# Optimization experiments

Hardware: AMD Instinct MI355X
Metric: run time of the kernel (lower is better)

Reference implementation:

```python
import jax, jax.numpy as jnp
import numpy as np


def _gru_scan(x_seq, Wih, Whh, bih, bhh):
    # x_seq: (S, N, D); PyTorch GRU/GRUCell gate math, h0 = 0. Returns (S, N, H).
    H = Whh.shape[1]
    gi_all = x_seq @ Wih.T + bih  # precompute input projections: (S, N, 3H)

    def step(h, gi):
        gh = h @ Whh.T + bhh
        ir, iz, inn = jnp.split(gi, 3, axis=-1)
        hr, hz, hn = jnp.split(gh, 3, axis=-1)
        r = jax.nn.sigmoid(ir + hr)
        z = jax.nn.sigmoid(iz + hz)
        n = jnp.tanh(inn + r * hn)
        h_new = (1.0 - z) * n + z * h
        return h_new, h_new

    h0 = jnp.zeros((x_seq.shape[1], H), x_seq.dtype)
    _, ys = jax.lax.scan(step, h0, gi_all)
    return ys


def setup_inputs() -> dict:
    key = jax.random.key(0)
    ks = jax.random.split(key, 40)
    B, T = 32, 800
    NOTE, E, P, H0, H1, FE, RE = 128, 256, 256, 512, 512, 64, 64

    def w(k, shape):
        return jax.random.normal(k, shape, dtype=jnp.float32) * 0.05

    return {
        "note": jax.random.randint(ks[0], (B, T), 0, NOTE, dtype=jnp.int64),
        "f0_prev": jax.random.normal(ks[1], (B, T), dtype=jnp.float32),
        "rmse_prev": jax.random.normal(ks[2], (B, T), dtype=jnp.float32),
        "note_emb": w(ks[3], (NOTE, E)),
        "f0_W": w(ks[4], (FE, 1)), "f0_b": w(ks[5], (FE,)),
        "rmse_W": w(ks[6], (RE, 1)), "rmse_b": w(ks[7], (RE,)),
        "pre1_W": w(ks[8], (P, E)), "pre1_b": w(ks[9], (P,)),
        "pre2_W": w(ks[10], (P, P)), "pre2_b": w(ks[11], (P,)),
        "encf_Wih": w(ks[12], (3 * H0, P)), "encf_Whh": w(ks[13], (3 * H0, H0)),
        "encf_bih": w(ks[14], (3 * H0,)), "encf_bhh": w(ks[15], (3 * H0,)),
        "encb_Wih": w(ks[16], (3 * H0, P)), "encb_Whh": w(ks[17], (3 * H0, H0)),
        "encb_bih": w(ks[18], (3 * H0,)), "encb_bhh": w(ks[19], (3 * H0,)),
        "decf_Wih": w(ks[20], (3 * H1, 2 * H0 + FE)), "decf_Whh": w(ks[21], (3 * H1, H1)),
        "decf_bih": w(ks[22], (3 * H1,)), "decf_bhh": w(ks[23], (3 * H1,)),
        "decr_Wih": w(ks[24], (3 * H1, 2 * H0 + RE)), "decr_Whh": w(ks[25], (3 * H1, H1)),
        "decr_bih": w(ks[26], (3 * H1,)), "decr_bhh": w(ks[27], (3 * H1,)),
        "postf_W": w(ks[28], (1, H1)), "postf_b": w(ks[29], (1,)),
        "postr_W": w(ks[30], (1, H1)), "postr_b": w(ks[31], (1,)),
    }


def reference(note, f0_prev, rmse_prev, note_emb, f0_W, f0_b, rmse_W, rmse_b,
              pre1_W, pre1_b, pre2_W, pre2_b,
              encf_Wih, encf_Whh, encf_bih, encf_bhh,
              encb_Wih, encb_Whh, encb_bih, encb_bhh,
              decf_Wih, decf_Whh, decf_bih, decf_bhh,
              decr_Wih, decr_Whh, decr_bih, decr_bhh,
              postf_W, postf_b, postr_W, postr_b):
    # Embeddings. Linear(1, FE) on a [B,T] signal == outer-broadcast with W[:,0].
    ne = note_emb[note]                                   # (B, T, E)
    f0e = f0_prev[..., None] * f0_W[:, 0] + f0_b          # (B, T, FE)
    rme = rmse_prev[..., None] * rmse_W[:, 0] + rmse_b    # (B, T, RE)

    # Prenet: Linear -> Tanh -> Linear -> Tanh
    h = jnp.tanh(jnp.tanh(ne @ pre1_W.T + pre1_b) @ pre2_W.T + pre2_b)  # (B, T, P)

    # Encoder: torch nn.GRU built WITHOUT batch_first and called with lengths=None,
    # so the recurrence runs over axis 0 (B) with T acting as the GRU batch. Replicated.
    ef = _gru_scan(h, encf_Wih, encf_Whh, encf_bih, encf_bhh)            # (B, T, H0)
    eb = _gru_scan(h[::-1], encb_Wih, encb_Whh, encb_bih, encb_bhh)[::-1]
    enc = jnp.concatenate([ef, eb], axis=-1)                             # (B, T, 2H0)

    # Decoders: GRUCell loop over T with teacher forcing (y_prevs has T>1 steps),
    # so step-t input is concat(enc[:, t], embed(prev[:, t])) -> standard scan.
    xt = jnp.transpose(enc, (1, 0, 2))                                   # (T, B, 2H0)
    hf = _gru_scan(jnp.concatenate([xt, jnp.transpose(f0e, (1, 0, 2))], -1),
                   decf_Wih, decf_Whh, decf_bih, decf_bhh)               # (T, B, H1)
    hr = _gru_scan(jnp.concatenate([xt, jnp.transpose(rme, (1, 0, 2))], -1),
                   decr_Wih, decr_Whh, decr_bih, decr_bhh)               # (T, B, H1)

    f0 = jnp.transpose((hf @ postf_W.T + postf_b)[..., 0], (1, 0))       # (B, T)
    rmse = jnp.transpose((hr @ postr_W.T + postr_b)[..., 0], (1, 0))     # (B, T)
    return (f0, rmse)
```

## Files before the change

kernel.cpp:

```cpp
#include <hip/hip_runtime.h>
#include <hip/hip_bf16.h>


typedef __bf16 bf16;
typedef bf16 bf16x8 __attribute__((ext_vector_type(8)));
typedef float f32x4 __attribute__((ext_vector_type(4)));
typedef float f32x2 __attribute__((ext_vector_type(2)));

#define BATCH 32
#define TLEN 800
#define BT (BATCH * TLEN)

__device__ __forceinline__ float bf2f(bf16 v) {
    unsigned short u = __builtin_bit_cast(unsigned short, v);
    unsigned int x = ((unsigned int)u) << 16;
    return __builtin_bit_cast(float, x);
}
__device__ __forceinline__ bf16 f2bf(float f) {
    unsigned int x = __builtin_bit_cast(unsigned int, f);
    unsigned int r = (x + 0x7FFFu + ((x >> 16) & 1u)) >> 16;
    return __builtin_bit_cast(bf16, (unsigned short)r);
}
__device__ __forceinline__ bf16x8 ld8f(const float* p) {
    f32x4 a = *(const f32x4*)p;
    f32x4 b = *(const f32x4*)(p + 4);
    bf16x8 r;
#pragma unroll
    for (int i = 0; i < 4; i++) {
        r[i] = f2bf(a[i]);
        r[i + 4] = f2bf(b[i]);
    }
    return r;
}
__device__ __forceinline__ void splitv(f32x4 a, f32x4 b, bf16x8& vh, bf16x8& vl) {
#pragma unroll
    for (int j = 0; j < 4; j++) {
        bf16 h0 = f2bf(a[j]);
        vh[j] = h0;
        vl[j] = f2bf(a[j] - bf2f(h0));
        bf16 h1 = f2bf(b[j]);
        vh[j + 4] = h1;
        vl[j + 4] = f2bf(b[j] - bf2f(h1));
    }
}
__device__ __forceinline__ f32x4 mfma16(bf16x8 a, bf16x8 b, f32x4 c) {
    return __builtin_amdgcn_mfma_f32_16x16x32_bf16(a, b, c, 0, 0, 0);
}
__device__ __forceinline__ float sigm(float x) { return 1.f / (1.f + __expf(-x)); }

__device__ __forceinline__ void cst_f32(float* p, float v) {
    __hip_atomic_store((unsigned int*)p, __builtin_bit_cast(unsigned int, v),
                       __ATOMIC_RELAXED, __HIP_MEMORY_SCOPE_AGENT);
}
__device__ __forceinline__ float cld_f32(const float* p) {
    unsigned int u = __hip_atomic_load((const unsigned int*)p, __ATOMIC_RELAXED,
                                       __HIP_MEMORY_SCOPE_AGENT);
    return __builtin_bit_cast(float, u);
}
__device__ __forceinline__ f32x4 cld_f32x4(const float* p) {
    unsigned long long a = __hip_atomic_load((const unsigned long long*)p,
                                             __ATOMIC_RELAXED,
                                             __HIP_MEMORY_SCOPE_AGENT);
    unsigned long long b = __hip_atomic_load((const unsigned long long*)(p + 2),
                                             __ATOMIC_RELAXED,
                                             __HIP_MEMORY_SCOPE_AGENT);
    f32x2 fa = __builtin_bit_cast(f32x2, a);
    f32x2 fb = __builtin_bit_cast(f32x2, b);
    f32x4 r;
    r[0] = fa[0]; r[1] = fa[1]; r[2] = fb[0]; r[3] = fb[1];
    return r;
}

template <int MODE>
__global__ __launch_bounds__(256) void gemm01_k(
    const int* __restrict__ note, const float* __restrict__ asrc,
    const float* __restrict__ W, const float* __restrict__ bias,
    float* __restrict__ out, int t0, int TC) {
    __shared__ bf16 Ah[128][72], Al[128][72], Bs[128][72];

    const int tid = threadIdx.x;
    const int lane = tid & 63, wv = tid >> 6;
    const int wm = wv & 1, wn = wv >> 1;
    const int l15 = lane & 15, hi = lane >> 4;
    const int bm = blockIdx.x * 128, bn = blockIdx.y * 128;
    const int ch = (tid & 7) * 8, arow = tid >> 3;

    f32x4 acc[4][4] = {};
    const float* ap[4];
    if (MODE == 0) {
        int zc = 0;
        for (int i = 0; i < 64; i++) zc += (note[2 * i + 1] == 0) ? 1 : 0;
        const bool n64 = (zc >= 60);
#pragma unroll
        for (int i = 0; i < 4; i++) {
            int m = bm + arow + 32 * i;
            int b = m / TC, tt = m - b * TC;
            int idx = b * TLEN + t0 + tt;
            int id = n64 ? note[2 * idx] : note[idx];
            id = id < 0 ? 0 : (id > 127 ? 127 : id);
            ap[i] = asrc + (size_t)id * 256;
        }
    } else {
#pragma unroll
        for (int i = 0; i < 4; i++) ap[i] = asrc + (size_t)(bm + arow + 32 * i) * 256;
    }

    for (int k0 = 0; k0 < 256; k0 += 64) {
#pragma unroll
        for (int i = 0; i < 4; i++) {
            int row = arow + 32 * i;
            f32x4 va = *(const f32x4*)(ap[i] + k0 + ch);
            f32x4 vb = *(const f32x4*)(ap[i] + k0 + ch + 4);
            bf16x8 vh, vl;
            splitv(va, vb, vh, vl);
            *(bf16x8*)&Ah[row][ch] = vh;
            *(bf16x8*)&Al[row][ch] = vl;
        }
#pragma unroll
        for (int i = 0; i < 4; i++) {
            int row = arow + 32 * i;
            *(bf16x8*)&Bs[row][ch] = ld8f(W + (size_t)(bn + row) * 256 + k0 + ch);
        }
        __syncthreads();
#pragma unroll
        for (int kk = 0; kk < 64; kk += 32) {
            bf16x8 ah[4], al[4], bb[4];
#pragma unroll
            for (int mt = 0; mt < 4; mt++) {
                ah[mt] = *(const bf16x8*)&Ah[wm * 64 + mt * 16 + l15][kk + hi * 8];
                al[mt] = *(const bf16x8*)&Al[wm * 64 + mt * 16 + l15][kk + hi * 8];
            }
#pragma unroll
            for (int nt = 0; nt < 4; nt++)
                bb[nt] = *(const bf16x8*)&Bs[wn * 64 + nt * 16 + l15][kk + hi * 8];
#pragma unroll
            for (int mt = 0; mt < 4; mt++)
#pragma unroll
                for (int nt = 0; nt < 4; nt++) {
                    acc[mt][nt] = mfma16(ah[mt], bb[nt], acc[mt][nt]);
                    acc[mt][nt] = mfma16(al[mt], bb[nt], acc[mt][nt]);
                }
        }
        __syncthreads();
    }

#pragma unroll
    for (int mt = 0; mt < 4; mt++)
#pragma unroll
        for (int nt = 0; nt < 4; nt++) {
            int n = bn + wn * 64 + nt * 16 + l15;
            float bs = bias[n];
#pragma unroll
            for (int r = 0; r < 4; r++) {
                int m = bm + wm * 64 + mt * 16 + hi * 4 + r;
                out[(size_t)m * 256 + n] = tanhf(acc[mt][nt][r] + bs);
            }
        }
}

__global__ __launch_bounds__(256) void gemm2_k(
    const float* __restrict__ ef, const float* __restrict__ eb,
    const float* __restrict__ sig, const float* __restrict__ sigW,
    const float* __restrict__ sigB, const float* __restrict__ W,
    const float* __restrict__ bias, float* __restrict__ out, int t0, int TC) {
    __shared__ bf16 Ah[128][72], Al[128][72];
    __shared__ bf16 Bh[64][72], Bl[64][72];

    const int tid = threadIdx.x;
    const int lane = tid & 63, wv = tid >> 6;
    const int wm = wv & 1, wn = wv >> 1;
    const int l15 = lane & 15, hi = lane >> 4;
    const int bm = blockIdx.x * 128, bn = blockIdx.y * 64;
    const int ch = (tid & 7) * 8, arow = tid >> 3;

    f32x4 acc[4][2] = {};
    int rb[4];
    float sigv[4];
#pragma unroll
    for (int i = 0; i < 4; i++) {
        int m = bm + arow + 32 * i;
        int tt = m >> 5, b = m & 31;
        rb[i] = b * TC + tt;
        sigv[i] = sig[b * TLEN + t0 + tt];
    }

    for (int k0 = 0; k0 < 1088; k0 += 64) {
#pragma unroll
        for (int i = 0; i < 4; i++) {
            int row = arow + 32 * i;
            int k = k0 + ch;
            f32x4 va, vb;
            if (k < 512) {
                va = *(const f32x4*)(ef + (size_t)rb[i] * 512 + k);
                vb = *(const f32x4*)(ef + (size_t)rb[i] * 512 + k + 4);
            } else if (k < 1024) {
                va = *(const f32x4*)(eb + (size_t)rb[i] * 512 + (k - 512));
                vb = *(const f32x4*)(eb + (size_t)rb[i] * 512 + (k - 512) + 4);
            } else {
                f32x4 w0 = *(const f32x4*)(sigW + ch);
                f32x4 w1 = *(const f32x4*)(sigW + ch + 4);
                f32x4 b0 = *(const f32x4*)(sigB + ch);
                f32x4 b1 = *(const f32x4*)(sigB + ch + 4);
                float s = sigv[i];
#pragma unroll
                for (int j = 0; j < 4; j++) {
                    va[j] = s * w0[j] + b0[j];
                    vb[j] = s * w1[j] + b1[j];
                }
            }
            bf16x8 vh, vl;
            splitv(va, vb, vh, vl);
            *(bf16x8*)&Ah[row][ch] = vh;
            *(bf16x8*)&Al[row][ch] = vl;
        }
#pragma unroll
        for (int i = 0; i < 2; i++) {
            int row = arow + 32 * i;
            const float* src = W + (size_t)(bn + row) * 1088 + k0 + ch;
            f32x4 va = *(const f32x4*)src;
            f32x4 vb = *(const f32x4*)(src + 4);
            bf16x8 vh, vl;
            splitv(va, vb, vh, vl);
            *(bf16x8*)&Bh[row][ch] = vh;
            *(bf16x8*)&Bl[row][ch] = vl;
        }
        __syncthreads();
#pragma unroll
        for (int kk = 0; kk < 64; kk += 32) {
            bf16x8 ah[4], al[4], bh[2], bl[2];
#pragma unroll
            for (int mt = 0; mt < 4; mt++) {
                ah[mt] = *(const bf16x8*)&Ah[wm * 64 + mt * 16 + l15][kk + hi * 8];
                al[mt] = *(const bf16x8*)&Al[wm * 64 + mt * 16 + l15][kk + hi * 8];
            }
#pragma unroll
            for (int nt = 0; nt < 2; nt++) {
                bh[nt] = *(const bf16x8*)&Bh[wn * 32 + nt * 16 + l15][kk + hi * 8];
                bl[nt] = *(const bf16x8*)&Bl[wn * 32 + nt * 16 + l15][kk + hi * 8];
            }
#pragma unroll
            for (int mt = 0; mt < 4; mt++)
#pragma unroll
                for (int nt = 0; nt < 2; nt++) {
                    acc[mt][nt] = mfma16(ah[mt], bh[nt], acc[mt][nt]);
                    acc[mt][nt] = mfma16(al[mt], bh[nt], acc[mt][nt]);
                    acc[mt][nt] = mfma16(ah[mt], bl[nt], acc[mt][nt]);
                }
        }
        __syncthreads();
    }

#pragma unroll
    for (int mt = 0; mt < 4; mt++)
#pragma unroll
        for (int nt = 0; nt < 2; nt++) {
            int n = bn + wn * 32 + nt * 16 + l15;
            float bs = bias[n];
#pragma unroll
            for (int r = 0; r < 4; r++) {
                int m = bm + wm * 64 + mt * 16 + hi * 4 + r;
                out[(size_t)m * 1536 + n] = acc[mt][nt][r] + bs;
            }
        }
}

__global__ __launch_bounds__(256) void enc_step_k(
    int step, int TC, const float* __restrict__ hpre, float* __restrict__ efb,
    float* __restrict__ ebb, const float* __restrict__ fWih,
    const float* __restrict__ fWhh, const float* __restrict__ fbih,
    const float* __restrict__ fbhh, const float* __restrict__ bWih,
    const float* __restrict__ bWhh, const float* __restrict__ bbih,
    const float* __restrict__ bbhh) {
    __shared__ bf16 As[32][72], Alo[32][72];
    __shared__ bf16 Bs[96][72], Blo[96][72];

    const int dir = blockIdx.z;
    const float* Wih = dir ? bWih : fWih;
    const float* Whh = dir ? bWhh : fWhh;
    const float* bih = dir ? bbih : fbih;
    const float* bhh = dir ? bbhh : fbhh;
    float* outb = dir ? ebb : efb;
    const int bsrc = dir ? (31 - step) : step;
    const int prevb = dir ? (32 - step) : (step - 1);

    const int tid = threadIdx.x;
    const int lane = tid & 63, wv = tid >> 6;
    const int mt = wv & 1, jt = wv >> 1;
    const int l15 = lane & 15, hi = lane >> 4;
    const int mtile = blockIdx.x, jtile = blockIdx.y;
    const int ch = (tid & 7) * 8, arow = tid >> 3;

    f32x4 acc_r = {}, acc_z = {}, acc_in = {}, acc_hn = {};

    const int nblocks = (step == 0) ? 4 : 12;
    for (int kb = 0; kb < nblocks; kb++) {
        int k0 = kb * 64;
        {
            int trow = mtile * 32 + arow;
            int tcl = trow < TC ? trow : TC - 1;
            const float* src = (k0 < 256)
                                   ? (hpre + ((size_t)bsrc * TC + tcl) * 256 + k0 + ch)
                                   : (outb + ((size_t)prevb * TC + tcl) * 512 + (k0 - 256) + ch);
            f32x4 va = *(const f32x4*)src;
            f32x4 vb = *(const f32x4*)(src + 4);
            bf16x8 vh, vl;
            splitv(va, vb, vh, vl);
            *(bf16x8*)&As[arow][ch] = vh;
            *(bf16x8*)&Alo[arow][ch] = vl;
        }
#pragma unroll
        for (int i = 0; i < 3; i++) {
            int row = arow + 32 * i;
            int s = row >> 5, j = row & 31;
            int wr = s * 512 + jtile * 32 + j;
            const float* src = (k0 < 256) ? (Wih + (size_t)wr * 256 + k0 + ch)
                                          : (Whh + (size_t)wr * 512 + (k0 - 256) + ch);
            f32x4 va = *(const f32x4*)src;
            f32x4 vb = *(const f32x4*)(src + 4);
            bf16x8 vh, vl;
            splitv(va, vb, vh, vl);
            *(bf16x8*)&Bs[row][ch] = vh;
            *(bf16x8*)&Blo[row][ch] = vl;
        }
        __syncthreads();
#pragma unroll
        for (int kk = 0; kk < 64; kk += 32) {
            bf16x8 a = *(const bf16x8*)&As[mt * 16 + l15][kk + hi * 8];
            bf16x8 alo = *(const bf16x8*)&Alo[mt * 16 + l15][kk + hi * 8];
            bf16x8 brh = *(const bf16x8*)&Bs[jt * 16 + l15][kk + hi * 8];
            bf16x8 brl = *(const bf16x8*)&Blo[jt * 16 + l15][kk + hi * 8];
            bf16x8 bzh = *(const bf16x8*)&Bs[32 + jt * 16 + l15][kk + hi * 8];
            bf16x8 bzl = *(const bf16x8*)&Blo[32 + jt * 16 + l15][kk + hi * 8];
            bf16x8 bnh = *(const bf16x8*)&Bs[64 + jt * 16 + l15][kk + hi * 8];
            bf16x8 bnl = *(const bf16x8*)&Blo[64 + jt * 16 + l15][kk + hi * 8];
            acc_r = mfma16(a, brh, acc_r);
            acc_r = mfma16(alo, brh, acc_r);
            acc_r = mfma16(a, brl, acc_r);
            acc_z = mfma16(a, bzh, acc_z);
            acc_z = mfma16(alo, bzh, acc_z);
            acc_z = mfma16(a, bzl, acc_z);
            if (k0 < 256) {
                acc_in = mfma16(a, bnh, acc_in);
                acc_in = mfma16(alo, bnh, acc_in);
                acc_in = mfma16(a, bnl, acc_in);
            } else {
                acc_hn = mfma16(a, bnh, acc_hn);
                acc_hn = mfma16(alo, bnh, acc_hn);
                acc_hn = mfma16(a, bnl, acc_hn);
            }
        }
        __syncthreads();
    }

    int j = jtile * 32 + jt * 16 + l15;
    float bir = bih[j] + bhh[j];
    float biz = bih[512 + j] + bhh[512 + j];
    float bin = bih[1024 + j];
    float bhn = bhh[1024 + j];
#pragma unroll
    for (int r = 0; r < 4; r++) {
        int trow = mtile * 32 + mt * 16 + hi * 4 + r;
        if (trow < TC) {
            float rr = sigm(acc_r[r] + bir);
            float zz = sigm(acc_z[r] + biz);
            float nn = tanhf(acc_in[r] + bin + rr * (acc_hn[r] + bhn));
            float hp = (step > 0) ? outb[((size_t)prevb * TC + trow) * 512 + j] : 0.f;
            outb[((size_t)bsrc * TC + trow) * 512 + j] = (1.f - zz) * nn + zz * hp;
        }
    }
}

__global__ __launch_bounds__(256, 1) void dec_k(
    const float* __restrict__ giF, const float* __restrict__ giR,
    const float* __restrict__ WhhF, const float* __restrict__ WhhR,
    const float* __restrict__ bhhF, const float* __restrict__ bhhR,
    float* __restrict__ HcurF, float* __restrict__ HcurR,
    const float* __restrict__ HprevF, const float* __restrict__ HprevR,
    int* __restrict__ flags, int t0, int TC) {
    const int d = blockIdx.x >> 4;
    const int g = blockIdx.x & 15;
    const float* gi = d ? giR : giF;
    const float* Whh = d ? WhhR : WhhF;
    const float* bhh = d ? bhhR : bhhF;
    float* Hcur = d ? HcurR : HcurF;
    const float* Hprev = d ? HprevR : HprevF;
    int* flg = flags + d * 16;

    const int tid = threadIdx.x;
    const int lane = tid & 63, wv = tid >> 6;
    const int mt = wv & 1, jt = wv >> 1;
    const int l15 = lane & 15, hi = lane >> 4;
    const int j_abs = g * 32 + jt * 16 + l15;

    bf16x8 Wf[3][16];
#pragma unroll
    for (int s = 0; s < 3; s++)
#pragma unroll
        for (int kb = 0; kb < 16; kb++)
            Wf[s][kb] = ld8f(Whh + (size_t)(s * 512 + j_abs) * 512 + kb * 32 + hi * 8);

    const float bhr = bhh[j_abs];
    const float bhz = bhh[512 + j_abs];
    const float bhn = bhh[1024 + j_abs];

    float hpreg[4] = {0.f, 0.f, 0.f, 0.f};

    for (int tt = 0; tt < TC; tt++) {
        const int t = t0 + tt;
        float gr[4], gz[4], gn[4];
#pragma unroll
        for (int r = 0; r < 4; r++) {
            int b = mt * 16 + hi * 4 + r;
            const float* gp = gi + ((size_t)tt * BATCH + b) * 1536 + j_abs;
            gr[r] = gp[0];
            gz[r] = gp[512];
            gn[r] = gp[1024];
        }

        f32x4 ar = {}, az = {}, an = {};
        float hp[4] = {0.f, 0.f, 0.f, 0.f};
        if (t > 0) {
            const float* base;
            if (tt > 0) {
                if (wv == 0 && lane < 16) {
                    while (__hip_atomic_load(&flg[lane], __ATOMIC_RELAXED,
                                             __HIP_MEMORY_SCOPE_AGENT) < t)
                        __builtin_amdgcn_s_sleep(1);
                }
                __syncthreads();
                base = Hcur + (size_t)(tt - 1) * BATCH * 512;
            } else {
                base = Hprev + (size_t)(TC - 1) * BATCH * 512;
            }
            const float* ap = base + (size_t)(mt * 16 + l15) * 512 + hi * 8;
#pragma unroll
            for (int half = 0; half < 2; half++) {
                f32x4 raw[8][2];
#pragma unroll
                for (int q = 0; q < 8; q++) {
                    int kb = half * 8 + q;
                    raw[q][0] = cld_f32x4(ap + kb * 32);
                    raw[q][1] = cld_f32x4(ap + kb * 32 + 4);
                }
#pragma unroll
                for (int q = 0; q < 8; q++) {
                    int kb = half * 8 + q;
                    bf16x8 ah, al;
                    splitv(raw[q][0], raw[q][1], ah, al);
                    ar = mfma16(ah, Wf[0][kb], ar);
                    ar = mfma16(al, Wf[0][kb], ar);
                    az = mfma16(ah, Wf[1][kb], az);
                    az = mfma16(al, Wf[1][kb], az);
                    an = mfma16(ah, Wf[2][kb], an);
                    an = mfma16(al, Wf[2][kb], an);
                }
            }
            if (tt > 0) {
#pragma unroll
                for (int r = 0; r < 4; r++) hp[r] = hpreg[r];
            } else {
#pragma unroll
                for (int r = 0; r < 4; r++) {
                    int b = mt * 16 + hi * 4 + r;
                    hp[r] = cld_f32(base + (size_t)b * 512 + j_abs);
                }
            }
        }
#pragma unroll
        for (int r = 0; r < 4; r++) {
            int b = mt * 16 + hi * 4 + r;
            float rr = sigm(gr[r] + ar[r] + bhr);
            float zz = sigm(gz[r] + az[r] + bhz);
            float nn = tanhf(gn[r] + rr * (an[r] + bhn));
            float hnew = (1.f - zz) * nn + zz * hp[r];
            cst_f32(&Hcur[((size_t)tt * BATCH + b) * 512 + j_abs], hnew);
            hpreg[r] = hnew;
        }
        __syncthreads();
        if (tid == 0)
            __hip_atomic_store(&flg[g], t + 1, __ATOMIC_RELAXED,
                               __HIP_MEMORY_SCOPE_AGENT);
    }
}

__global__ __launch_bounds__(256) void post_k(
    const float* __restrict__ H, const float* __restrict__ W,
    const float* __restrict__ bs, float* __restrict__ out, int t0) {
    const int wv = threadIdx.x >> 6, lane = threadIdx.x & 63;
    const int row = blockIdx.x * 4 + wv;
    const int tt = row >> 5, b = row & 31;
    const float bias = bs[0];
    const float* hp = H + (size_t)row * 512 + lane * 8;
    f32x4 h0 = *(const f32x4*)hp;
    f32x4 h1 = *(const f32x4*)(hp + 4);
    f32x4 w0 = *(const f32x4*)(W + lane * 8);
    f32x4 w1 = *(const f32x4*)(W + lane * 8 + 4);
    float s = 0.f;
#pragma unroll
    for (int i = 0; i < 4; i++) s += h0[i] * w0[i] + h1[i] * w1[i];
#pragma unroll
    for (int off = 32; off > 0; off >>= 1) s += __shfl_down(s, off);
    if (lane == 0) out[b * TLEN + t0 + tt] = s + bias;
}

__global__ void zero_k(int* __restrict__ flags) {
    int i = blockIdx.x * 256 + threadIdx.x;
    if (i < 2 * TLEN) flags[i] = 0;
}

extern "C" void kernel_launch(void* const* d_in, const int* in_sizes, int n_in,
                              void* d_out, int out_size, void* d_ws, size_t ws_size,
                              hipStream_t stream) {
    const int* note = (const int*)d_in[0];
    const float* f0_prev = (const float*)d_in[1];
    const float* rmse_prev = (const float*)d_in[2];
    const float* note_emb = (const float*)d_in[3];
    const float* f0_W = (const float*)d_in[4];
    const float* f0_b = (const float*)d_in[5];
    const float* rmse_W = (const float*)d_in[6];
    const float* rmse_b = (const float*)d_in[7];
    const float* pre1_W = (const float*)d_in[8];
    const float* pre1_b = (const float*)d_in[9];
    const float* pre2_W = (const float*)d_in[10];
    const float* pre2_b = (const float*)d_in[11];
    const float* encf_Wih = (const float*)d_in[12];
    const float* encf_Whh = (const float*)d_in[13];
    const float* encf_bih = (const float*)d_in[14];
    const float* encf_bhh = (const float*)d_in[15];
    const float* encb_Wih = (const float*)d_in[16];
    const float* encb_Whh = (const float*)d_in[17];
    const float* encb_bih = (const float*)d_in[18];
    const float* encb_bhh = (const float*)d_in[19];
    const float* decf_Wih = (const float*)d_in[20];
    const float* decf_Whh = (const float*)d_in[21];
    const float* decf_bih = (const float*)d_in[22];
    const float* decf_bhh = (const float*)d_in[23];
    const float* decr_Wih = (const float*)d_in[24];
    const float* decr_Whh = (const float*)d_in[25];
    const float* decr_bih = (const float*)d_in[26];
    const float* decr_bhh = (const float*)d_in[27];
    const float* postf_W = (const float*)d_in[28];
    const float* postf_b = (const float*)d_in[29];
    const float* postr_W = (const float*)d_in[30];
    const float* postr_b = (const float*)d_in[31];
    float* out = (float*)d_out;

    const int tcs[9] = {800, 400, 200, 100, 80, 40, 20, 8, 4};
    int TC = 4;
    for (int i = 0; i < 9; i++) {
        int tc = tcs[i];
        int slots = (tc == TLEN) ? 1 : 2;
        size_t need = (size_t)(2 * 65536 + 2 * 196608 + 2 * slots * 65536) * tc + 65536;
        if (ws_size >= need) { TC = tc; break; }
    }
    const int NC = TLEN / TC;
    const int slots = (NC == 1) ? 1 : 2;

    char* ws = (char*)d_ws;
    size_t off = 0;
    auto carve = [&](size_t bytes) {
        void* p = ws + off;
        off += (bytes + 255) & ~(size_t)255;
        return p;
    };
    const size_t slotB = (size_t)65536 * TC;
    float* ef_c = (float*)carve(slotB);
    float* eb_c = (float*)carve(slotB);
    float* giF_c = (float*)carve((size_t)196608 * TC);
    float* giR_c = (float*)carve((size_t)196608 * TC);
    float* ringF = (float*)carve(slotB * slots);
    float* ringR = (float*)carve(slotB * slots);
    int* flags = (int*)carve(2 * TLEN * 4);
    float* t1_c = giF_c;
    float* hpre_c = giF_c + (size_t)8192 * TC;

    zero_k<<<dim3(7), 256, 0, stream>>>(flags);

    const size_t slotE = (size_t)TC * BATCH * 512;

    for (int c = 0; c < NC; c++) {
        const int t0 = c * TC;
        const int mg = TC * 32 / 128;

        gemm01_k<0><<<dim3(mg, 2), 256, 0, stream>>>(note, note_emb, pre1_W, pre1_b,
                                                     t1_c, t0, TC);
        gemm01_k<1><<<dim3(mg, 2), 256, 0, stream>>>(nullptr, t1_c, pre2_W, pre2_b,
                                                     hpre_c, t0, TC);
        const int etiles = (TC + 31) / 32;
        for (int i = 0; i < 32; i++)
            enc_step_k<<<dim3(etiles, 16, 2), 256, 0, stream>>>(
                i, TC, hpre_c, ef_c, eb_c, encf_Wih, encf_Whh, encf_bih, encf_bhh,
                encb_Wih, encb_Whh, encb_bih, encb_bhh);

        gemm2_k<<<dim3(mg, 24), 256, 0, stream>>>(ef_c, eb_c, f0_prev, f0_W, f0_b,
                                                  decf_Wih, decf_bih, giF_c, t0, TC);
        gemm2_k<<<dim3(mg, 24), 256, 0, stream>>>(ef_c, eb_c, rmse_prev, rmse_W,
                                                  rmse_b, decr_Wih, decr_bih, giR_c,
                                                  t0, TC);

        float* HcurF = ringF + (size_t)(c & (slots - 1)) * slotE;
        const float* HprevF = ringF + (size_t)((c - 1) & (slots - 1)) * slotE;
        float* HcurR = ringR + (size_t)(c & (slots - 1)) * slotE;
        const float* HprevR = ringR + (size_t)((c - 1) & (slots - 1)) * slotE;

        dec_k<<<dim3(32), 256, 0, stream>>>(giF_c, giR_c, decf_Whh, decr_Whh,
                                            decf_bhh, decr_bhh, HcurF, HcurR,
                                            HprevF, HprevR, flags, t0, TC);

        post_k<<<dim3(TC * 32 / 4), 256, 0, stream>>>(HcurF, postf_W, postf_b,
                                                      out, t0);
        post_k<<<dim3(TC * 32 / 4), 256, 0, stream>>>(HcurR, postr_W, postr_b,
                                                      out + BT, t0);
    }
    (void)in_sizes; (void)n_in; (void)out_size; (void)ws_size;
}
```

Measured before the change: 12.00 ms.

## Fuse encoder GRU steps into one persistent scan kernel with pre-split weights

The 32 per-step encoder launches are replaced by one scan kernel per direction and time tile. The scan loops over all 32 batch steps and keeps the hidden state in registers and LDS. The input projection is hoisted out of the recurrence into a bulk GEMM (new MODE 2 of gemm01_k), and Whh is pre-split once into bf16 hi/lo copies so the per-step fp32-to-bf16 conversion goes away. Scratch buffers are reassigned to the ring slots, and the workspace requirement grows by the split weights. The cost is heavy weight re-reading from global memory inside each step and low parallelism per block.

```diff
diff --git a/kernel.cpp b/kernel.cpp
--- a/kernel.cpp
+++ b/kernel.cpp
@@ -6,6 +6,7 @@
 typedef bf16 bf16x8 __attribute__((ext_vector_type(8)));
 typedef float f32x4 __attribute__((ext_vector_type(4)));
 typedef float f32x2 __attribute__((ext_vector_type(2)));
+typedef unsigned int u32x4 __attribute__((ext_vector_type(4)));
 
 #define BATCH 32
 #define TLEN 800
@@ -70,6 +71,17 @@
     r[0] = fa[0]; r[1] = fa[1]; r[2] = fb[0]; r[3] = fb[1];
     return r;
 }
+__device__ __forceinline__ void unpk8(const unsigned int v[8], bf16x8& ah,
+                                      bf16x8& al) {
+    u32x4 hw, lw;
+#pragma unroll
+    for (int i = 0; i < 4; i++) {
+        hw[i] = __builtin_amdgcn_perm(v[2 * i + 1], v[2 * i], 0x07060302u);
+        lw[i] = __builtin_amdgcn_perm(v[2 * i + 1], v[2 * i], 0x05040100u);
+    }
+    ah = __builtin_bit_cast(bf16x8, hw);
+    al = __builtin_bit_cast(bf16x8, lw);
+}
 
 template <int MODE>
 __global__ __launch_bounds__(256) void gemm01_k(
@@ -84,6 +96,7 @@
     const int l15 = lane & 15, hi = lane >> 4;
     const int bm = blockIdx.x * 128, bn = blockIdx.y * 128;
     const int ch = (tid & 7) * 8, arow = tid >> 3;
+    const int LDC = (MODE == 2) ? 1536 : 256;
 
     f32x4 acc[4][4] = {};
     const float* ap[4];
@@ -149,11 +162,12 @@
 #pragma unroll
         for (int nt = 0; nt < 4; nt++) {
             int n = bn + wn * 64 + nt * 16 + l15;
-            float bs = bias[n];
+            float bs = (MODE == 2) ? 0.f : bias[n];
 #pragma unroll
             for (int r = 0; r < 4; r++) {
                 int m = bm + wm * 64 + mt * 16 + hi * 4 + r;
-                out[(size_t)m * 256 + n] = tanhf(acc[mt][nt][r] + bs);
+                float v = acc[mt][nt][r] + bs;
+                out[(size_t)m * LDC + n] = (MODE == 2) ? v : tanhf(v);
             }
         }
 }
@@ -264,109 +278,128 @@
         }
 }
 
-__global__ __launch_bounds__(256) void enc_step_k(
-    int step, int TC, const float* __restrict__ hpre, float* __restrict__ efb,
-    float* __restrict__ ebb, const float* __restrict__ fWih,
-    const float* __restrict__ fWhh, const float* __restrict__ fbih,
-    const float* __restrict__ fbhh, const float* __restrict__ bWih,
-    const float* __restrict__ bWhh, const float* __restrict__ bbih,
+__global__ __launch_bounds__(256) void wsplit_k(const float* __restrict__ fWhh,
+                                                const float* __restrict__ bWhh,
+                                                bf16* __restrict__ out) {
+    const int idx = (blockIdx.x * 256 + threadIdx.x) * 8;
+    const int dir = blockIdx.y;
+    const float* src = dir ? bWhh : fWhh;
+    bf16* oh = out + (size_t)dir * 2 * 786432;
+    bf16* ol = oh + 786432;
+    f32x4 a = *(const f32x4*)(src + idx);
+    f32x4 b = *(const f32x4*)(src + idx + 4);
+    bf16x8 vh, vl;
+    splitv(a, b, vh, vl);
+    *(bf16x8*)(oh + idx) = vh;
+    *(bf16x8*)(ol + idx) = vl;
+}
+
+__global__ __launch_bounds__(256, 1) void enc_scan_k(
+    int TC, const float* __restrict__ egiF, const float* __restrict__ egiB,
+    float* __restrict__ efb, float* __restrict__ ebb,
+    const bf16* __restrict__ wsp, const float* __restrict__ fbih,
+    const float* __restrict__ fbhh, const float* __restrict__ bbih,
     const float* __restrict__ bbhh) {
-    __shared__ bf16 As[32][72], Alo[32][72];
-    __shared__ bf16 Bs[96][72], Blo[96][72];
-
-    const int dir = blockIdx.z;
-    const float* Wih = dir ? bWih : fWih;
-    const float* Whh = dir ? bWhh : fWhh;
+    __shared__ unsigned int Apk[16][516];
+
+    const int dir = blockIdx.y;
+    const float* egi = dir ? egiB : egiF;
+    float* outb = dir ? ebb : efb;
+    const bf16* Wh = wsp + (size_t)dir * 2 * 786432;
+    const bf16* Wl = Wh + 786432;
     const float* bih = dir ? bbih : fbih;
     const float* bhh = dir ? bbhh : fbhh;
-    float* outb = dir ? ebb : efb;
-    const int bsrc = dir ? (31 - step) : step;
-    const int prevb = dir ? (32 - step) : (step - 1);
 
     const int tid = threadIdx.x;
-    const int lane = tid & 63, wv = tid >> 6;
-    const int mt = wv & 1, jt = wv >> 1;
+    const int lane = tid & 63, w = tid >> 6;
     const int l15 = lane & 15, hi = lane >> 4;
-    const int mtile = blockIdx.x, jtile = blockIdx.y;
-    const int ch = (tid & 7) * 8, arow = tid >> 3;
-
-    f32x4 acc_r = {}, acc_z = {}, acc_in = {}, acc_hn = {};
-
-    const int nblocks = (step == 0) ? 4 : 12;
-    for (int kb = 0; kb < nblocks; kb++) {
-        int k0 = kb * 64;
-        {
-            int trow = mtile * 32 + arow;
-            int tcl = trow < TC ? trow : TC - 1;
-            const float* src = (k0 < 256)
-                                   ? (hpre + ((size_t)bsrc * TC + tcl) * 256 + k0 + ch)
-                                   : (outb + ((size_t)prevb * TC + tcl) * 512 + (k0 - 256) + ch);
-            f32x4 va = *(const f32x4*)src;
-            f32x4 vb = *(const f32x4*)(src + 4);
-            bf16x8 vh, vl;
-            splitv(va, vb, vh, vl);
-            *(bf16x8*)&As[arow][ch] = vh;
-            *(bf16x8*)&Alo[arow][ch] = vl;
-        }
-#pragma unroll
-        for (int i = 0; i < 3; i++) {
-            int row = arow + 32 * i;
-            int s = row >> 5, j = row & 31;
-            int wr = s * 512 + jtile * 32 + j;
-            const float* src = (k0 < 256) ? (Wih + (size_t)wr * 256 + k0 + ch)
-                                          : (Whh + (size_t)wr * 512 + (k0 - 256) + ch);
-            f32x4 va = *(const f32x4*)src;
-            f32x4 vb = *(const f32x4*)(src + 4);
-            bf16x8 vh, vl;
-            splitv(va, vb, vh, vl);
-            *(bf16x8*)&Bs[row][ch] = vh;
-            *(bf16x8*)&Blo[row][ch] = vl;
+    const int ttile = blockIdx.x;
+
+    float bir[8], biz[8], bin[8], bhn[8];
+#pragma unroll
+    for (int q = 0; q < 8; q++) {
+        int j = w * 128 + q * 16 + l15;
+        bir[q] = bih[j] + bhh[j];
+        biz[q] = bih[512 + j] + bhh[512 + j];
+        bin[q] = bih[1024 + j];
+        bhn[q] = bhh[1024 + j];
+    }
+    int trow[4];
+#pragma unroll
+    for (int r = 0; r < 4; r++) {
+        int tr = ttile * 16 + hi * 4 + r;
+        trow[r] = tr < TC ? tr : TC - 1;
+    }
+
+    f32x4 hold[8];
+#pragma unroll
+    for (int q = 0; q < 8; q++) hold[q] = f32x4{0.f, 0.f, 0.f, 0.f};
+
+    for (int b = 0; b < 32; b++) {
+        const int bsrc = dir ? (31 - b) : b;
+        f32x4 acc_r[8], acc_z[8], acc_hn[8];
+#pragma unroll
+        for (int q = 0; q < 8; q++) {
+            int j = w * 128 + q * 16 + l15;
+#pragma unroll
+            for (int r = 0; r < 4; r++) {
+                const float* ep = egi + ((size_t)bsrc * TC + trow[r]) * 1536 + j;
+                acc_r[q][r] = ep[0];
+                acc_z[q][r] = ep[512];
+            }
+            acc_hn[q] = f32x4{0.f, 0.f, 0.f, 0.f};
+        }
+        if (b > 0) {
+            for (int kb = 0; kb < 16; kb++) {
+                u32x4 qa = *(const u32x4*)&Apk[l15][kb * 32 + hi * 8];
+                u32x4 qb = *(const u32x4*)&Apk[l15][kb * 32 + hi * 8 + 4];
+                unsigned int v[8] = {qa[0], qa[1], qa[2], qa[3],
+                                     qb[0], qb[1], qb[2], qb[3]};
+                bf16x8 ah, al;
+                unpk8(v, ah, al);
+#pragma unroll
+                for (int q = 0; q < 8; q++) {
+                    int jw = w * 128 + q * 16 + l15;
+                    const size_t ko = (size_t)kb * 32 + hi * 8;
+                    bf16x8 brh = *(const bf16x8*)(Wh + (size_t)jw * 512 + ko);
+                    bf16x8 brl = *(const bf16x8*)(Wl + (size_t)jw * 512 + ko);
+                    bf16x8 bzh = *(const bf16x8*)(Wh + (size_t)(512 + jw) * 512 + ko);
+                    bf16x8 bzl = *(const bf16x8*)(Wl + (size_t)(512 + jw) * 512 + ko);
+                    bf16x8 bnh = *(const bf16x8*)(Wh + (size_t)(1024 + jw) * 512 + ko);
+                    bf16x8 bnl = *(const bf16x8*)(Wl + (size_t)(1024 + jw) * 512 + ko);
+                    acc_r[q] = mfma16(ah, brh, acc_r[q]);
+                    acc_r[q] = mfma16(al, brh, acc_r[q]);
+                    acc_r[q] = mfma16(ah, brl, acc_r[q]);
+                    acc_z[q] = mfma16(ah, bzh, acc_z[q]);
+                    acc_z[q] = mfma16(al, bzh, acc_z[q]);
+                    acc_z[q] = mfma16(ah, bzl, acc_z[q]);
+                    acc_hn[q] = mfma16(ah, bnh, acc_hn[q]);
+                    acc_hn[q] = mfma16(al, bnh, acc_hn[q]);
+                    acc_hn[q] = mfma16(ah, bnl, acc_hn[q]);
+                }
+            }
         }
         __syncthreads();
 #pragma unroll
-        for (int kk = 0; kk < 64; kk += 32) {
-            bf16x8 a = *(const bf16x8*)&As[mt * 16 + l15][kk + hi * 8];
-            bf16x8 alo = *(const bf16x8*)&Alo[mt * 16 + l15][kk + hi * 8];
-            bf16x8 brh = *(const bf16x8*)&Bs[jt * 16 + l15][kk + hi * 8];
-            bf16x8 brl = *(const bf16x8*)&Blo[jt * 16 + l15][kk + hi * 8];
-            bf16x8 bzh = *(const bf16x8*)&Bs[32 + jt * 16 + l15][kk + hi * 8];
-            bf16x8 bzl = *(const bf16x8*)&Blo[32 + jt * 16 + l15][kk + hi * 8];
-            bf16x8 bnh = *(const bf16x8*)&Bs[64 + jt * 16 + l15][kk + hi * 8];
-            bf16x8 bnl = *(const bf16x8*)&Blo[64 + jt * 16 + l15][kk + hi * 8];
-            acc_r = mfma16(a, brh, acc_r);
-            acc_r = mfma16(alo, brh, acc_r);
-            acc_r = mfma16(a, brl, acc_r);
-            acc_z = mfma16(a, bzh, acc_z);
-            acc_z = mfma16(alo, bzh, acc_z);
-            acc_z = mfma16(a, bzl, acc_z);
-            if (k0 < 256) {
-                acc_in = mfma16(a, bnh, acc_in);
-                acc_in = mfma16(alo, bnh, acc_in);
-                acc_in = mfma16(a, bnl, acc_in);
-            } else {
-                acc_hn = mfma16(a, bnh, acc_hn);
-                acc_hn = mfma16(alo, bnh, acc_hn);
-                acc_hn = mfma16(a, bnl, acc_hn);
+        for (int q = 0; q < 8; q++) {
+            int j = w * 128 + q * 16 + l15;
+#pragma unroll
+            for (int r = 0; r < 4; r++) {
+                float gin = egi[((size_t)bsrc * TC + trow[r]) * 1536 + 1024 + j];
+                float rr = sigm(acc_r[q][r] + bir[q]);
+                float zz = sigm(acc_z[q][r] + biz[q]);
+                float nn = tanhf(gin + bin[q] + rr * (acc_hn[q][r] + bhn[q]));
+                float hnew = (1.f - zz) * nn + zz * hold[q][r];
+                hold[q][r] = hnew;
+                outb[((size_t)bsrc * TC + trow[r]) * 512 + j] = hnew;
+                bf16 hh = f2bf(hnew);
+                bf16 hl = f2bf(hnew - bf2f(hh));
+                Apk[hi * 4 + r][j] =
+                    ((unsigned int)__builtin_bit_cast(unsigned short, hh) << 16) |
+                    (unsigned int)__builtin_bit_cast(unsigned short, hl);
             }
         }
         __syncthreads();
-    }
-
-    int j = jtile * 32 + jt * 16 + l15;
-    float bir = bih[j] + bhh[j];
-    float biz = bih[512 + j] + bhh[512 + j];
-    float bin = bih[1024 + j];
-    float bhn = bhh[1024 + j];
-#pragma unroll
-    for (int r = 0; r < 4; r++) {
-        int trow = mtile * 32 + mt * 16 + hi * 4 + r;
-        if (trow < TC) {
-            float rr = sigm(acc_r[r] + bir);
-            float zz = sigm(acc_z[r] + biz);
-            float nn = tanhf(acc_in[r] + bin + rr * (acc_hn[r] + bhn));
-            float hp = (step > 0) ? outb[((size_t)prevb * TC + trow) * 512 + j] : 0.f;
-            outb[((size_t)bsrc * TC + trow) * 512 + j] = (1.f - zz) * nn + zz * hp;
-        }
     }
 }
 
@@ -505,7 +538,9 @@
 
 __global__ void zero_k(int* __restrict__ flags) {
     int i = blockIdx.x * 256 + threadIdx.x;
-    if (i < 2 * TLEN) flags[i] = 0;
+    if (i < 2 * TLEN)
+        __hip_atomic_store(&flags[i], 0, __ATOMIC_RELAXED,
+                           __HIP_MEMORY_SCOPE_AGENT);
 }
 
 extern "C" void kernel_launch(void* const* d_in, const int* in_sizes, int n_in,
@@ -550,7 +585,8 @@
     for (int i = 0; i < 9; i++) {
         int tc = tcs[i];
         int slots = (tc == TLEN) ? 1 : 2;
-        size_t need = (size_t)(2 * 65536 + 2 * 196608 + 2 * slots * 65536) * tc + 65536;
+        size_t need = (size_t)(2 * 65536 + 2 * 196608 + 2 * slots * 65536) * tc +
+                      6291456 + 131072;
         if (ws_size >= need) { TC = tc; break; }
     }
     const int NC = TLEN / TC;
@@ -570,27 +606,38 @@
     float* giR_c = (float*)carve((size_t)196608 * TC);
     float* ringF = (float*)carve(slotB * slots);
     float* ringR = (float*)carve(slotB * slots);
+    bf16* wsp = (bf16*)carve(6291456);
     int* flags = (int*)carve(2 * TLEN * 4);
-    float* t1_c = giF_c;
-    float* hpre_c = giF_c + (size_t)8192 * TC;
+
+    float* egiF = giF_c;
+    float* egiB = giR_c;
 
     zero_k<<<dim3(7), 256, 0, stream>>>(flags);
+    wsplit_k<<<dim3(384, 2), 256, 0, stream>>>(encf_Whh, encb_Whh, wsp);
 
     const size_t slotE = (size_t)TC * BATCH * 512;
 
     for (int c = 0; c < NC; c++) {
         const int t0 = c * TC;
         const int mg = TC * 32 / 128;
+        const int cs = c & (slots - 1), ps = (c - 1) & (slots - 1);
+
+        float* t1_c = ringF + (size_t)cs * slotE;
+        float* hpre_c = ringR + (size_t)cs * slotE;
 
         gemm01_k<0><<<dim3(mg, 2), 256, 0, stream>>>(note, note_emb, pre1_W, pre1_b,
                                                      t1_c, t0, TC);
         gemm01_k<1><<<dim3(mg, 2), 256, 0, stream>>>(nullptr, t1_c, pre2_W, pre2_b,
                                                      hpre_c, t0, TC);
-        const int etiles = (TC + 31) / 32;
-        for (int i = 0; i < 32; i++)
-            enc_step_k<<<dim3(etiles, 16, 2), 256, 0, stream>>>(
-                i, TC, hpre_c, ef_c, eb_c, encf_Wih, encf_Whh, encf_bih, encf_bhh,
-                encb_Wih, encb_Whh, encb_bih, encb_bhh);
+        gemm01_k<2><<<dim3(mg, 12), 256, 0, stream>>>(nullptr, hpre_c, encf_Wih,
+                                                      nullptr, egiF, t0, TC);
+        gemm01_k<2><<<dim3(mg, 12), 256, 0, stream>>>(nullptr, hpre_c, encb_Wih,
+                                                      nullptr, egiB, t0, TC);
+
+        const int ttiles = (TC + 15) / 16;
+        enc_scan_k<<<dim3(ttiles, 2), 256, 0, stream>>>(
+            TC, egiF, egiB, ef_c, eb_c, wsp, encf_bih, encf_bhh, encb_bih,
+            encb_bhh);
 
         gemm2_k<<<dim3(mg, 24), 256, 0, stream>>>(ef_c, eb_c, f0_prev, f0_W, f0_b,
                                                   decf_Wih, decf_bih, giF_c, t0, TC);
@@ -598,10 +645,10 @@
                                                   rmse_b, decr_Wih, decr_bih, giR_c,
                                                   t0, TC);
 
-        float* HcurF = ringF + (size_t)(c & (slots - 1)) * slotE;
-        const float* HprevF = ringF + (size_t)((c - 1) & (slots - 1)) * slotE;
-        float* HcurR = ringR + (size_t)(c & (slots - 1)) * slotE;
-        const float* HprevR = ringR + (size_t)((c - 1) & (slots - 1)) * slotE;
+        float* HcurF = ringF + (size_t)cs * slotE;
+        const float* HprevF = ringF + (size_t)ps * slotE;
+        float* HcurR = ringR + (size_t)cs * slotE;
+        const float* HprevR = ringR + (size_t)ps * slotE;
 
         dec_k<<<dim3(32), 256, 0, stream>>>(giF_c, giR_c, decf_Whh, decr_Whh,
                                             decf_bhh, decr_bhh, HcurF, HcurR,
```

After: 21.34 ms. +77.9%, slower.
